# Performance work log

Measured on AMD Instinct MI355X. Metric: run time of the kernel, lower is better.

Reference implementation:

```python
import jax, jax.numpy as jnp
import numpy as np

POOLED = 7      # pooled_size
KSIZE = 2       # kernel_size (max-pool window & stride)
CROP = POOLED * KSIZE  # crop_and_resize crop_size = 14


def setup_inputs() -> dict:
    key = jax.random.key(0)
    k1, k2 = jax.random.split(key)
    feature_maps = jax.random.normal(k1, (2, 50, 50, 512), dtype=jnp.float32)
    # normalized boxes in [x1, y1, x2, y2] order (the layer swaps to y1,x1,y2,x2);
    # tf.image.crop_and_resize handles arbitrary (even inverted) boxes, so raw
    # uniforms are valid inputs.
    rois = jax.random.uniform(k2, (2, 128, 4), dtype=jnp.float32)
    return {"feature_maps": feature_maps, "rois": rois}


def _roi_pool(feature_maps, rois):
    B, H, W, C = feature_maps.shape
    R = rois.shape[1]
    N = B * R
    # [x1,y1,x2,y2] -> [y1,x1,y2,x2] as in the layer
    boxes = rois.reshape(N, 4)[:, jnp.array([1, 0, 3, 2])]
    y1, x1, y2, x2 = boxes[:, 0], boxes[:, 1], boxes[:, 2], boxes[:, 3]
    bidx = jnp.repeat(jnp.arange(B), R)  # box_indices, [N]

    # tf.image.crop_and_resize sample grid (crop_size > 1 branch)
    i = jnp.arange(CROP, dtype=feature_maps.dtype)
    ys = y1[:, None] * (H - 1) + i[None, :] * ((y2 - y1)[:, None] * (H - 1) / (CROP - 1))  # [N,S]
    xs = x1[:, None] * (W - 1) + i[None, :] * ((x2 - x1)[:, None] * (W - 1) / (CROP - 1))  # [N,S]
    valid_y = (ys >= 0) & (ys <= H - 1)
    valid_x = (xs >= 0) & (xs <= W - 1)

    y0f = jnp.floor(ys)
    x0f = jnp.floor(xs)
    wy = (ys - y0f)[:, :, None, None]   # [N,S,1,1]
    wx = (xs - x0f)[:, None, :, None]   # [N,1,S,1]
    y0i = jnp.clip(y0f.astype(jnp.int32), 0, H - 1)
    y1i = jnp.clip(y0i + 1, 0, H - 1)
    x0i = jnp.clip(x0f.astype(jnp.int32), 0, W - 1)
    x1i = jnpp = None
    x1i = jnp.clip(x0i + 1, 0, W - 1)

    # gather the two bilinear rows per sample line: [N, S, W, C]
    rows0 = feature_maps[bidx[:, None], y0i]
    rows1 = feature_maps[bidx[:, None], y1i]
    rows = rows0 + (rows1 - rows0) * wy  # lerp in y

    # gather the two columns and lerp in x: [N, S, S, C]
    v0 = jnp.take_along_axis(rows, x0i[:, None, :, None], axis=2)
    v1 = jnp.take_along_axis(rows, x1i[:, None, :, None], axis=2)
    crops = v0 + (v1 - v0) * wx

    # out-of-range samples -> extrapolation_value = 0 (TF default)
    valid = valid_y[:, :, None, None] & valid_x[:, None, :, None]
    crops = jnp.where(valid, crops, jnp.zeros((), crops.dtype))

    # 2x2/stride-2 max pool -> [N, POOLED, POOLED, C]
    pooled = crops.reshape(N, POOLED, KSIZE, POOLED, KSIZE, C).max(axis=(2, 4))
    return pooled


def reference(feature_maps, rois):
    # flatten=False, keep_batch_dim=False -> [batch*num_rois, pooled, pooled, C]
    return _roi_pool(feature_maps, rois)
```

## Files before the change

kernel.cpp:

```cpp
#include <hip/hip_runtime.h>
#include <hip/hip_fp16.h>


constexpr int H = 50, W = 50, C = 512;
constexpr int POOLEDX = 7, KSIZE = 2, CROP = 14;
constexpr int RPB = 128;
constexpr int NXCD = 8;
constexpr int PIX = POOLEDX * POOLEDX;
constexpr int NROI = 2 * RPB;
constexpr int ROIS_PER_XCD = NROI / NXCD;
constexpr int NELEM = 2 * H * W * C;

__global__ __launch_bounds__(256) void cvt_kernel(
    const float* __restrict__ in, __half* __restrict__ out)
{
    const int i = (blockIdx.x * 256 + threadIdx.x) * 8;
    const float4* in4 = reinterpret_cast<const float4*>(in + i);
    const float4 a = in4[0];
    const float4 b = in4[1];
    __half h[8];
    h[0] = __float2half(a.x); h[1] = __float2half(a.y);
    h[2] = __float2half(a.z); h[3] = __float2half(a.w);
    h[4] = __float2half(b.x); h[5] = __float2half(b.y);
    h[6] = __float2half(b.z); h[7] = __float2half(b.w);
    *reinterpret_cast<float4*>(out + i) = *reinterpret_cast<const float4*>(h);
}

__global__ __launch_bounds__(64) void roi_pool_kernel(
    const __half* __restrict__ fmh,
    const float* __restrict__ rois,
    float* __restrict__ out)
{
    const int hw   = blockIdx.x;
    const int xcd  = hw & (NXCD - 1);
    const int slot = hw >> 3;
    const int n    = xcd * ROIS_PER_XCD + slot / PIX;
    const int k    = slot % PIX;
    const int ph   = k / POOLEDX;
    const int pw   = k % POOLEDX;
    const int b    = n / RPB;
    const int t    = threadIdx.x;

    const float4* __restrict__ fm4 = reinterpret_cast<const float4*>(fmh);

    const float x1 = rois[n * 4 + 0];
    const float y1 = rois[n * 4 + 1];
    const float x2 = rois[n * 4 + 2];
    const float y2 = rois[n * 4 + 3];

    const float ybase = y1 * (float)(H - 1);
    const float xbase = x1 * (float)(W - 1);
    const float ystep = (y2 - y1) * (float)(H - 1) / (float)(CROP - 1);
    const float xstep = (x2 - x1) * (float)(W - 1) / (float)(CROP - 1);

    const int fmbase = b * H * W;

    int   x0i[KSIZE], x1i[KSIZE];
    float wx[KSIZE];
    bool  vx[KSIZE];
    #pragma unroll
    for (int kx = 0; kx < KSIZE; ++kx) {
        const int   ix = pw * KSIZE + kx;
        const float xs = xbase + (float)ix * xstep;
        vx[kx] = (xs >= 0.0f) && (xs <= (float)(W - 1));
        const float x0f = floorf(xs);
        wx[kx] = xs - x0f;
        int xi = (int)x0f;
        xi = min(max(xi, 0), W - 1);
        x0i[kx] = xi;
        x1i[kx] = min(xi + 1, W - 1);
    }

    float acc[8];
    #pragma unroll
    for (int c = 0; c < 8; ++c) acc[c] = -__builtin_inff();

    #pragma unroll
    for (int ky = 0; ky < KSIZE; ++ky) {
        const int   iy = ph * KSIZE + ky;
        const float ys = ybase + (float)iy * ystep;
        const bool  vy = (ys >= 0.0f) && (ys <= (float)(H - 1));
        const float y0f = floorf(ys);
        const float wy  = ys - y0f;
        int y0i = (int)y0f;
        y0i = min(max(y0i, 0), H - 1);
        const int y1i = min(y0i + 1, H - 1);

        #pragma unroll
        for (int kx = 0; kx < KSIZE; ++kx) {
            const int p00 = (fmbase + y0i * W + x0i[kx]) * (C / 8) + t;
            const int p01 = (fmbase + y0i * W + x1i[kx]) * (C / 8) + t;
            const int p10 = (fmbase + y1i * W + x0i[kx]) * (C / 8) + t;
            const int p11 = (fmbase + y1i * W + x1i[kx]) * (C / 8) + t;

            const float4 r00 = fm4[p00];
            const float4 r01 = fm4[p01];
            const float4 r10 = fm4[p10];
            const float4 r11 = fm4[p11];

            const __half2* h00 = reinterpret_cast<const __half2*>(&r00);
            const __half2* h01 = reinterpret_cast<const __half2*>(&r01);
            const __half2* h10 = reinterpret_cast<const __half2*>(&r10);
            const __half2* h11 = reinterpret_cast<const __half2*>(&r11);

            const bool valid = vx[kx] && vy;
            const float wxk = wx[kx];

            #pragma unroll
            for (int q = 0; q < 4; ++q) {
                const float2 f00 = __half22float2(h00[q]);
                const float2 f01 = __half22float2(h01[q]);
                const float2 f10 = __half22float2(h10[q]);
                const float2 f11 = __half22float2(h11[q]);

                float vA, vB;
                {
                    const float r0 = f00.x + (f10.x - f00.x) * wy;
                    const float r1 = f01.x + (f11.x - f01.x) * wy;
                    vA = r0 + (r1 - r0) * wxk;
                }
                {
                    const float r0 = f00.y + (f10.y - f00.y) * wy;
                    const float r1 = f01.y + (f11.y - f01.y) * wy;
                    vB = r0 + (r1 - r0) * wxk;
                }
                if (!valid) { vA = 0.0f; vB = 0.0f; }
                acc[2 * q]     = fmaxf(acc[2 * q],     vA);
                acc[2 * q + 1] = fmaxf(acc[2 * q + 1], vB);
            }
        }
    }

    const int oblk = n * PIX + ph * POOLEDX + pw;
    float4* __restrict__ out4 = reinterpret_cast<float4*>(out);
    const int obase = oblk * (C / 4) + t * 2;
    float4 o0, o1;
    o0.x = acc[0]; o0.y = acc[1]; o0.z = acc[2]; o0.w = acc[3];
    o1.x = acc[4]; o1.y = acc[5]; o1.z = acc[6]; o1.w = acc[7];
    out4[obase]     = o0;
    out4[obase + 1] = o1;
}

extern "C" void kernel_launch(void* const* d_in, const int* in_sizes, int n_in,
                              void* d_out, int out_size, void* d_ws, size_t ws_size,
                              hipStream_t stream) {
    const float* fm   = (const float*)d_in[0];
    const float* rois = (const float*)d_in[1];
    float* out  = (float*)d_out;
    __half* fmh = (__half*)d_ws;

    cvt_kernel<<<NELEM / (256 * 8), 256, 0, stream>>>(fm, fmh);

    const int nblocks = NROI * PIX;
    roi_pool_kernel<<<nblocks, 64, 0, stream>>>(fmh, rois, out);
}
```

Measured before the change: 79.94 us.

## Stage feature-map rows in LDS per ROI channel slab and reuse across samples

Replaces the one-block-per-pooled-pixel kernel with one 256-thread block per ROI and 128-channel slab. The block walks the 14 sample rows, caches the two needed feature-map rows (restricted to the ROI's x-range) in a double-slot shared buffer tagged by row index, and reloads only rows it has not already cached. Each 16-thread group handles one sample column, and 2x2 pooling is done with a lane shuffle plus a row-pair accumulation. This removes redundant global gathers of the same rows across pooled pixels, but leaves only 1024 blocks and adds __syncthreads on every row reload, which may limit parallelism.

```diff
diff --git a/kernel.cpp b/kernel.cpp
--- a/kernel.cpp
+++ b/kernel.cpp
@@ -3,13 +3,14 @@
 
 
 constexpr int H = 50, W = 50, C = 512;
-constexpr int POOLEDX = 7, KSIZE = 2, CROP = 14;
+constexpr int POOLEDX = 7, CROP = 14;
 constexpr int RPB = 128;
-constexpr int NXCD = 8;
 constexpr int PIX = POOLEDX * POOLEDX;
 constexpr int NROI = 2 * RPB;
-constexpr int ROIS_PER_XCD = NROI / NXCD;
 constexpr int NELEM = 2 * H * W * C;
+constexpr int SLABCH = 128;
+constexpr int NSLAB  = C / SLABCH;
+constexpr int LSTR   = SLABCH + 8;
 
 __global__ __launch_bounds__(256) void cvt_kernel(
     const float* __restrict__ in, __half* __restrict__ out)
@@ -19,126 +20,143 @@
     const float4 a = in4[0];
     const float4 b = in4[1];
     __half h[8];
-    h[0] = __float2half(a.x); h[1] = __float2half(a.y);
-    h[2] = __float2half(a.z); h[3] = __float2half(a.w);
-    h[4] = __float2half(b.x); h[5] = __float2half(b.y);
-    h[6] = __float2half(b.z); h[7] = __float2half(b.w);
+    h[0]=__float2half(a.x); h[1]=__float2half(a.y); h[2]=__float2half(a.z); h[3]=__float2half(a.w);
+    h[4]=__float2half(b.x); h[5]=__float2half(b.y); h[6]=__float2half(b.z); h[7]=__float2half(b.w);
     *reinterpret_cast<float4*>(out + i) = *reinterpret_cast<const float4*>(h);
 }
 
-__global__ __launch_bounds__(64) void roi_pool_kernel(
+__global__ __launch_bounds__(256) void roi_pool_kernel(
     const __half* __restrict__ fmh,
     const float* __restrict__ rois,
     float* __restrict__ out)
 {
+    __shared__ __half lds[2][W][LSTR];
+
     const int hw   = blockIdx.x;
-    const int xcd  = hw & (NXCD - 1);
-    const int slot = hw >> 3;
-    const int n    = xcd * ROIS_PER_XCD + slot / PIX;
-    const int k    = slot % PIX;
-    const int ph   = k / POOLEDX;
-    const int pw   = k % POOLEDX;
-    const int b    = n / RPB;
+    const int n    = hw >> 2;
+    const int slab = hw & 3;
+    const int bat  = n / RPB;
     const int t    = threadIdx.x;
+    const int g    = t & 15;
+    const int j    = t >> 4;
 
-    const float4* __restrict__ fm4 = reinterpret_cast<const float4*>(fmh);
+    const float rx1 = rois[n*4+0], ry1 = rois[n*4+1];
+    const float rx2 = rois[n*4+2], ry2 = rois[n*4+3];
+    const float ybase = ry1 * 49.0f, xbase = rx1 * 49.0f;
+    const float ystep = ((ry2 - ry1) * 49.0f) / 13.0f;
+    const float xstep = ((rx2 - rx1) * 49.0f) / 13.0f;
 
-    const float x1 = rois[n * 4 + 0];
-    const float y1 = rois[n * 4 + 1];
-    const float x2 = rois[n * 4 + 2];
-    const float y2 = rois[n * 4 + 3];
+    const float xsA = xbase;
+    const float xsB = xbase + 13.0f * xstep;
+    int eA = (int)floorf(xsA); eA = min(max(eA, 0), W - 1);
+    int eB = (int)floorf(xsB); eB = min(max(eB, 0), W - 1);
+    const int xmin = min(eA, eB);
+    const int xmax = min(max(eA, eB) + 1, W - 1);
+    const int Wd   = xmax - xmin + 1;
 
-    const float ybase = y1 * (float)(H - 1);
-    const float xbase = x1 * (float)(W - 1);
-    const float ystep = (y2 - y1) * (float)(H - 1) / (float)(CROP - 1);
-    const float xstep = (x2 - x1) * (float)(W - 1) / (float)(CROP - 1);
+    float wx = 0.0f; bool vx = false; int c0 = 0, c1 = 0;
+    if (j < CROP) {
+        const float xsv = xbase + (float)j * xstep;
+        vx = (xsv >= 0.0f) && (xsv <= (float)(W - 1));
+        const float xfl = floorf(xsv);
+        wx = xsv - xfl;
+        int xi = (int)xfl; xi = min(max(xi, 0), W - 1);
+        c0 = xi - xmin;
+        c1 = min(xi + 1, W - 1) - xmin;
+    }
 
-    const int fmbase = b * H * W;
+    const __half* srcbase = fmh + ((long)bat * (H * W)) * C + slab * SLABCH + g * 8;
 
-    int   x0i[KSIZE], x1i[KSIZE];
-    float wx[KSIZE];
-    bool  vx[KSIZE];
-    #pragma unroll
-    for (int kx = 0; kx < KSIZE; ++kx) {
-        const int   ix = pw * KSIZE + kx;
-        const float xs = xbase + (float)ix * xstep;
-        vx[kx] = (xs >= 0.0f) && (xs <= (float)(W - 1));
-        const float x0f = floorf(xs);
-        wx[kx] = xs - x0f;
-        int xi = (int)x0f;
-        xi = min(max(xi, 0), W - 1);
-        x0i[kx] = xi;
-        x1i[kx] = min(xi + 1, W - 1);
-    }
+    int tag0 = -1, tag1 = -1;
 
     float acc[8];
     #pragma unroll
     for (int c = 0; c < 8; ++c) acc[c] = -__builtin_inff();
 
-    #pragma unroll
-    for (int ky = 0; ky < KSIZE; ++ky) {
-        const int   iy = ph * KSIZE + ky;
-        const float ys = ybase + (float)iy * ystep;
-        const bool  vy = (ys >= 0.0f) && (ys <= (float)(H - 1));
-        const float y0f = floorf(ys);
-        const float wy  = ys - y0f;
-        int y0i = (int)y0f;
-        y0i = min(max(y0i, 0), H - 1);
-        const int y1i = min(y0i + 1, H - 1);
+    for (int iy = 0; iy < CROP; ++iy) {
+        const float ysv = ybase + (float)iy * ystep;
+        const bool  vy  = (ysv >= 0.0f) && (ysv <= (float)(H - 1));
+        const float yfl = floorf(ysv);
+        const float wy  = ysv - yfl;
+        int ra = (int)yfl; ra = min(max(ra, 0), H - 1);
+        const int rb = min(ra + 1, H - 1);
+        const int sa = ra & 1, sb = rb & 1;
 
-        #pragma unroll
-        for (int kx = 0; kx < KSIZE; ++kx) {
-            const int p00 = (fmbase + y0i * W + x0i[kx]) * (C / 8) + t;
-            const int p01 = (fmbase + y0i * W + x1i[kx]) * (C / 8) + t;
-            const int p10 = (fmbase + y1i * W + x0i[kx]) * (C / 8) + t;
-            const int p11 = (fmbase + y1i * W + x1i[kx]) * (C / 8) + t;
+        const bool needA = ((sa ? tag1 : tag0) != ra);
+        const bool needB = (rb != ra) && ((sb ? tag1 : tag0) != rb);
+        if (needA || needB) {
+            __syncthreads();
+            if (needA) {
+                const __half* src = srcbase + (long)(ra * W + xmin) * C;
+                for (int px = j; px < Wd; px += 16)
+                    *reinterpret_cast<float4*>(&lds[sa][px][g * 8]) =
+                        *reinterpret_cast<const float4*>(src + (long)px * C);
+            }
+            if (needB) {
+                const __half* src = srcbase + (long)(rb * W + xmin) * C;
+                for (int px = j; px < Wd; px += 16)
+                    *reinterpret_cast<float4*>(&lds[sb][px][g * 8]) =
+                        *reinterpret_cast<const float4*>(src + (long)px * C);
+            }
+            if (sa) tag1 = ra; else tag0 = ra;
+            if (sb) tag1 = rb; else tag0 = rb;
+            __syncthreads();
+        }
 
-            const float4 r00 = fm4[p00];
-            const float4 r01 = fm4[p01];
-            const float4 r10 = fm4[p10];
-            const float4 r11 = fm4[p11];
-
-            const __half2* h00 = reinterpret_cast<const __half2*>(&r00);
-            const __half2* h01 = reinterpret_cast<const __half2*>(&r01);
-            const __half2* h10 = reinterpret_cast<const __half2*>(&r10);
-            const __half2* h11 = reinterpret_cast<const __half2*>(&r11);
-
-            const bool valid = vx[kx] && vy;
-            const float wxk = wx[kx];
-
+        if (j < CROP) {
+            const float4 ta0 = *reinterpret_cast<const float4*>(&lds[sa][c0][g * 8]);
+            const float4 ta1 = *reinterpret_cast<const float4*>(&lds[sa][c1][g * 8]);
+            const float4 tb0 = *reinterpret_cast<const float4*>(&lds[sb][c0][g * 8]);
+            const float4 tb1 = *reinterpret_cast<const float4*>(&lds[sb][c1][g * 8]);
+            const __half2* ha0 = reinterpret_cast<const __half2*>(&ta0);
+            const __half2* ha1 = reinterpret_cast<const __half2*>(&ta1);
+            const __half2* hb0 = reinterpret_cast<const __half2*>(&tb0);
+            const __half2* hb1 = reinterpret_cast<const __half2*>(&tb1);
+            const bool valid = vx && vy;
             #pragma unroll
             for (int q = 0; q < 4; ++q) {
-                const float2 f00 = __half22float2(h00[q]);
-                const float2 f01 = __half22float2(h01[q]);
-                const float2 f10 = __half22float2(h10[q]);
-                const float2 f11 = __half22float2(h11[q]);
-
+                const float2 fa0 = __half22float2(ha0[q]);
+                const float2 fa1 = __half22float2(ha1[q]);
+                const float2 fb0 = __half22float2(hb0[q]);
+                const float2 fb1 = __half22float2(hb1[q]);
                 float vA, vB;
                 {
-                    const float r0 = f00.x + (f10.x - f00.x) * wy;
-                    const float r1 = f01.x + (f11.x - f01.x) * wy;
-                    vA = r0 + (r1 - r0) * wxk;
+                    const float r0 = fa0.x + (fb0.x - fa0.x) * wy;
+                    const float r1 = fa1.x + (fb1.x - fa1.x) * wy;
+                    vA = r0 + (r1 - r0) * wx;
                 }
                 {
-                    const float r0 = f00.y + (f10.y - f00.y) * wy;
-                    const float r1 = f01.y + (f11.y - f01.y) * wy;
-                    vB = r0 + (r1 - r0) * wxk;
+                    const float r0 = fa0.y + (fb0.y - fa0.y) * wy;
+                    const float r1 = fa1.y + (fb1.y - fa1.y) * wy;
+                    vB = r0 + (r1 - r0) * wx;
                 }
                 if (!valid) { vA = 0.0f; vB = 0.0f; }
                 acc[2 * q]     = fmaxf(acc[2 * q],     vA);
                 acc[2 * q + 1] = fmaxf(acc[2 * q + 1], vB);
             }
         }
+
+        if (iy & 1) {
+            const int ph = iy >> 1;
+            float m[8];
+            #pragma unroll
+            for (int c = 0; c < 8; ++c) {
+                const float o = __shfl_xor(acc[c], 16, 64);
+                m[c] = fmaxf(acc[c], o);
+                acc[c] = -__builtin_inff();
+            }
+            if (((j & 1) == 0) && j < CROP) {
+                const int pw = j >> 1;
+                float* op = out + ((long)(n * PIX + ph * POOLEDX + pw) * C)
+                          + slab * SLABCH + g * 8;
+                float4 o0, o1;
+                o0.x = m[0]; o0.y = m[1]; o0.z = m[2]; o0.w = m[3];
+                o1.x = m[4]; o1.y = m[5]; o1.z = m[6]; o1.w = m[7];
+                *reinterpret_cast<float4*>(op)     = o0;
+                *reinterpret_cast<float4*>(op + 4) = o1;
+            }
+        }
     }
-
-    const int oblk = n * PIX + ph * POOLEDX + pw;
-    float4* __restrict__ out4 = reinterpret_cast<float4*>(out);
-    const int obase = oblk * (C / 4) + t * 2;
-    float4 o0, o1;
-    o0.x = acc[0]; o0.y = acc[1]; o0.z = acc[2]; o0.w = acc[3];
-    o1.x = acc[4]; o1.y = acc[5]; o1.z = acc[6]; o1.w = acc[7];
-    out4[obase]     = o0;
-    out4[obase + 1] = o1;
 }
 
 extern "C" void kernel_launch(void* const* d_in, const int* in_sizes, int n_in,
@@ -150,7 +168,5 @@
     __half* fmh = (__half*)d_ws;
 
     cvt_kernel<<<NELEM / (256 * 8), 256, 0, stream>>>(fm, fmh);
-
-    const int nblocks = NROI * PIX;
-    roi_pool_kernel<<<nblocks, 64, 0, stream>>>(fmh, rois, out);
+    roi_pool_kernel<<<NROI * NSLAB, 256, 0, stream>>>(fmh, rois, out);
 }
```

After: 98.32 us. 23.0% more time.

## Pack four ROI bins per block and do bilinear math in packed fp16

Applied to the files above, without the earlier changes.

Each 256-thread block now handles four pooled output pixels, one per wavefront, in place of one 64-thread block per pixel. The XCD-aware block-to-ROI swizzle is dropped for a linear task mapping. The bilinear interpolation and max now use 8-wide _Float16 vectors with precomputed corner weights, so packed half arithmetic replaces per-element fp32 conversion. This cuts ALU and conversion work and block count, but it loses precision because the whole interpolation runs in fp16, and it may lose the L2 locality the swizzle gave.

```diff
diff --git a/kernel.cpp b/kernel.cpp
--- a/kernel.cpp
+++ b/kernel.cpp
@@ -5,11 +5,12 @@
 constexpr int H = 50, W = 50, C = 512;
 constexpr int POOLEDX = 7, KSIZE = 2, CROP = 14;
 constexpr int RPB = 128;
-constexpr int NXCD = 8;
 constexpr int PIX = POOLEDX * POOLEDX;
 constexpr int NROI = 2 * RPB;
-constexpr int ROIS_PER_XCD = NROI / NXCD;
+constexpr int NTASK = NROI * PIX;
 constexpr int NELEM = 2 * H * W * C;
+
+typedef _Float16 h8 __attribute__((ext_vector_type(8)));
 
 __global__ __launch_bounds__(256) void cvt_kernel(
     const float* __restrict__ in, __half* __restrict__ out)
@@ -19,126 +20,95 @@
     const float4 a = in4[0];
     const float4 b = in4[1];
     __half h[8];
-    h[0] = __float2half(a.x); h[1] = __float2half(a.y);
-    h[2] = __float2half(a.z); h[3] = __float2half(a.w);
-    h[4] = __float2half(b.x); h[5] = __float2half(b.y);
-    h[6] = __float2half(b.z); h[7] = __float2half(b.w);
+    h[0]=__float2half(a.x); h[1]=__float2half(a.y); h[2]=__float2half(a.z); h[3]=__float2half(a.w);
+    h[4]=__float2half(b.x); h[5]=__float2half(b.y); h[6]=__float2half(b.z); h[7]=__float2half(b.w);
     *reinterpret_cast<float4*>(out + i) = *reinterpret_cast<const float4*>(h);
 }
 
-__global__ __launch_bounds__(64) void roi_pool_kernel(
+__global__ __launch_bounds__(256, 4) void roi_pool_kernel(
     const __half* __restrict__ fmh,
     const float* __restrict__ rois,
     float* __restrict__ out)
 {
-    const int hw   = blockIdx.x;
-    const int xcd  = hw & (NXCD - 1);
-    const int slot = hw >> 3;
-    const int n    = xcd * ROIS_PER_XCD + slot / PIX;
-    const int k    = slot % PIX;
-    const int ph   = k / POOLEDX;
-    const int pw   = k % POOLEDX;
-    const int b    = n / RPB;
-    const int t    = threadIdx.x;
+    const int task = blockIdx.x * 4 + (threadIdx.x >> 6);
+    const int lane = threadIdx.x & 63;
+    const int n  = task / PIX;
+    const int k  = task - n * PIX;
+    const int ph = k / POOLEDX;
+    const int pw = k - ph * POOLEDX;
+    const int bat = n / RPB;
 
-    const float4* __restrict__ fm4 = reinterpret_cast<const float4*>(fmh);
-
-    const float x1 = rois[n * 4 + 0];
-    const float y1 = rois[n * 4 + 1];
-    const float x2 = rois[n * 4 + 2];
-    const float y2 = rois[n * 4 + 3];
-
-    const float ybase = y1 * (float)(H - 1);
-    const float xbase = x1 * (float)(W - 1);
-    const float ystep = (y2 - y1) * (float)(H - 1) / (float)(CROP - 1);
-    const float xstep = (x2 - x1) * (float)(W - 1) / (float)(CROP - 1);
-
-    const int fmbase = b * H * W;
+    const float rx1 = rois[n*4+0], ry1 = rois[n*4+1];
+    const float rx2 = rois[n*4+2], ry2 = rois[n*4+3];
+    const float ybase = ry1 * (float)(H - 1);
+    const float xbase = rx1 * (float)(W - 1);
+    const float ystep = ((ry2 - ry1) * (float)(H - 1)) / (float)(CROP - 1);
+    const float xstep = ((rx2 - rx1) * (float)(W - 1)) / (float)(CROP - 1);
 
     int   x0i[KSIZE], x1i[KSIZE];
     float wx[KSIZE];
     bool  vx[KSIZE];
     #pragma unroll
     for (int kx = 0; kx < KSIZE; ++kx) {
-        const int   ix = pw * KSIZE + kx;
-        const float xs = xbase + (float)ix * xstep;
+        const float xs = xbase + (float)(pw * KSIZE + kx) * xstep;
         vx[kx] = (xs >= 0.0f) && (xs <= (float)(W - 1));
-        const float x0f = floorf(xs);
-        wx[kx] = xs - x0f;
-        int xi = (int)x0f;
-        xi = min(max(xi, 0), W - 1);
+        const float xf = floorf(xs);
+        wx[kx] = xs - xf;
+        int xi = (int)xf; xi = min(max(xi, 0), W - 1);
         x0i[kx] = xi;
         x1i[kx] = min(xi + 1, W - 1);
     }
 
-    float acc[8];
+    const __half* base = fmh + (long)bat * (H * W) * C + lane * 8;
+
+    h8 acc;
     #pragma unroll
-    for (int c = 0; c < 8; ++c) acc[c] = -__builtin_inff();
+    for (int c = 0; c < 8; ++c) acc[c] = (_Float16)(-60000.0f);
 
     #pragma unroll
     for (int ky = 0; ky < KSIZE; ++ky) {
-        const int   iy = ph * KSIZE + ky;
-        const float ys = ybase + (float)iy * ystep;
+        const float ys = ybase + (float)(ph * KSIZE + ky) * ystep;
         const bool  vy = (ys >= 0.0f) && (ys <= (float)(H - 1));
-        const float y0f = floorf(ys);
-        const float wy  = ys - y0f;
-        int y0i = (int)y0f;
-        y0i = min(max(y0i, 0), H - 1);
-        const int y1i = min(y0i + 1, H - 1);
+        const float yf = floorf(ys);
+        const float wy = ys - yf;
+        int y0 = (int)yf; y0 = min(max(y0, 0), H - 1);
+        const int y1 = min(y0 + 1, H - 1);
 
         #pragma unroll
         for (int kx = 0; kx < KSIZE; ++kx) {
-            const int p00 = (fmbase + y0i * W + x0i[kx]) * (C / 8) + t;
-            const int p01 = (fmbase + y0i * W + x1i[kx]) * (C / 8) + t;
-            const int p10 = (fmbase + y1i * W + x0i[kx]) * (C / 8) + t;
-            const int p11 = (fmbase + y1i * W + x1i[kx]) * (C / 8) + t;
+            const h8 t00 = *reinterpret_cast<const h8*>(base + (long)(y0 * W + x0i[kx]) * C);
+            const h8 t01 = *reinterpret_cast<const h8*>(base + (long)(y0 * W + x1i[kx]) * C);
+            const h8 t10 = *reinterpret_cast<const h8*>(base + (long)(y1 * W + x0i[kx]) * C);
+            const h8 t11 = *reinterpret_cast<const h8*>(base + (long)(y1 * W + x1i[kx]) * C);
 
-            const float4 r00 = fm4[p00];
-            const float4 r01 = fm4[p01];
-            const float4 r10 = fm4[p10];
-            const float4 r11 = fm4[p11];
+            const float wxk = wx[kx];
+            const _Float16 w00 = (_Float16)((1.0f - wy) * (1.0f - wxk));
+            const _Float16 w01 = (_Float16)((1.0f - wy) * wxk);
+            const _Float16 w10 = (_Float16)(wy * (1.0f - wxk));
+            const _Float16 w11 = (_Float16)(wy * wxk);
 
-            const __half2* h00 = reinterpret_cast<const __half2*>(&r00);
-            const __half2* h01 = reinterpret_cast<const __half2*>(&r01);
-            const __half2* h10 = reinterpret_cast<const __half2*>(&r10);
-            const __half2* h11 = reinterpret_cast<const __half2*>(&r11);
+            h8 v = t00 * w00 + t01 * w01 + t10 * w10 + t11 * w11;
 
-            const bool valid = vx[kx] && vy;
-            const float wxk = wx[kx];
+            if (!(vx[kx] && vy)) {
+                #pragma unroll
+                for (int c = 0; c < 8; ++c) v[c] = (_Float16)0.0f;
+            }
 
+#if __has_builtin(__builtin_elementwise_max)
+            acc = __builtin_elementwise_max(acc, v);
+#else
             #pragma unroll
-            for (int q = 0; q < 4; ++q) {
-                const float2 f00 = __half22float2(h00[q]);
-                const float2 f01 = __half22float2(h01[q]);
-                const float2 f10 = __half22float2(h10[q]);
-                const float2 f11 = __half22float2(h11[q]);
-
-                float vA, vB;
-                {
-                    const float r0 = f00.x + (f10.x - f00.x) * wy;
-                    const float r1 = f01.x + (f11.x - f01.x) * wy;
-                    vA = r0 + (r1 - r0) * wxk;
-                }
-                {
-                    const float r0 = f00.y + (f10.y - f00.y) * wy;
-                    const float r1 = f01.y + (f11.y - f01.y) * wy;
-                    vB = r0 + (r1 - r0) * wxk;
-                }
-                if (!valid) { vA = 0.0f; vB = 0.0f; }
-                acc[2 * q]     = fmaxf(acc[2 * q],     vA);
-                acc[2 * q + 1] = fmaxf(acc[2 * q + 1], vB);
-            }
+            for (int c = 0; c < 8; ++c) acc[c] = acc[c] > v[c] ? acc[c] : v[c];
+#endif
         }
     }
 
-    const int oblk = n * PIX + ph * POOLEDX + pw;
-    float4* __restrict__ out4 = reinterpret_cast<float4*>(out);
-    const int obase = oblk * (C / 4) + t * 2;
     float4 o0, o1;
-    o0.x = acc[0]; o0.y = acc[1]; o0.z = acc[2]; o0.w = acc[3];
-    o1.x = acc[4]; o1.y = acc[5]; o1.z = acc[6]; o1.w = acc[7];
-    out4[obase]     = o0;
-    out4[obase + 1] = o1;
+    o0.x = (float)acc[0]; o0.y = (float)acc[1]; o0.z = (float)acc[2]; o0.w = (float)acc[3];
+    o1.x = (float)acc[4]; o1.y = (float)acc[5]; o1.z = (float)acc[6]; o1.w = (float)acc[7];
+    float4* out4 = reinterpret_cast<float4*>(out) + (long)task * (C / 4) + lane * 2;
+    out4[0] = o0;
+    out4[1] = o1;
 }
 
 extern "C" void kernel_launch(void* const* d_in, const int* in_sizes, int n_in,
@@ -150,7 +120,5 @@
     __half* fmh = (__half*)d_ws;
 
     cvt_kernel<<<NELEM / (256 * 8), 256, 0, stream>>>(fm, fmh);
-
-    const int nblocks = NROI * PIX;
-    roi_pool_kernel<<<nblocks, 64, 0, stream>>>(fmh, rois, out);
+    roi_pool_kernel<<<NTASK / 4, 256, 0, stream>>>(fmh, rois, out);
 }
```

Result: no change. 79.79 us (-0.2%).
